# Performance work log

Measured on AMD Instinct MI355X. Metric: run time of the kernel, lower is better.

The kernel has to match this reference:

```python
import jax, jax.numpy as jnp
import numpy as np

MARGIN = 0.0
BINS = 10
ALPHA = 0.75
N = 16777216  # 2**24 pairs


def setup_inputs() -> dict:
    key = jax.random.key(0)
    k1, k2, k3 = jax.random.split(key, 3)
    output1 = jax.random.normal(k1, (N,), dtype=jnp.float32)
    output2 = jax.random.normal(k2, (N,), dtype=jnp.float32)
    target = jax.random.randint(k3, (N,), 0, 2, dtype=jnp.int64)
    return {"output1": output1, "output2": output2, "target": target}


def reference(output1, output2, target):
    dtype = output1.dtype
    t = target.astype(dtype)
    diff = output1 - output2
    # MarginRankingLoss(reduction='none'): max(0, -target*(x1-x2) + margin)
    loss = jnp.maximum(0.0, -t * diff + MARGIN)
    # gradient-norm proxy g in (0,1)
    expected_sign = 2.0 * t - 1.0
    g = jax.nn.sigmoid(-diff * expected_sign + MARGIN)
    g_norm = jnp.abs(g)
    edges = jnp.arange(BINS + 1, dtype=dtype) / BINS
    # histogram over BINS bins (fixed small loop over bins, vectorized over N)
    counts = jnp.stack([
        jnp.sum((g_norm >= edges[i]) & (g_norm < edges[i + 1]))
        for i in range(BINS)
    ]).astype(dtype)
    tot = jnp.clip(counts, 1.0)
    w = tot ** (-ALPHA)  # per-bin weight; constant wrt g in the original (.item() detaches)
    w = jax.lax.stop_gradient(w)
    bin_idx = jnp.clip(jnp.floor(g * BINS).astype(jnp.int32), 0, BINS - 1)
    sample_weights = w[bin_idx]
    return jnp.mean(loss * sample_weights)
```

## Files before the change

kernel.cpp:

```cpp
#include <hip/hip_runtime.h>

#define BINS 10
#define ALPHA 0.75f

constexpr int NB = 2048;
constexpr int NT = 256;

__global__ __launch_bounds__(NT) void ghm_pass1(
    const float* __restrict__ o1f, const float* __restrict__ o2f,
    const int* __restrict__ tgt, float* __restrict__ lsum_part,
    unsigned int* __restrict__ cnt_part, int n)
{
  const float4* o1 = reinterpret_cast<const float4*>(o1f);
  const float4* o2 = reinterpret_cast<const float4*>(o2f);
  const int4*   tg = reinterpret_cast<const int4*>(tgt);
  const int n4 = n >> 2;

  float ls[BINS];
  unsigned int c[BINS];
#pragma unroll
  for (int b = 0; b < BINS; ++b) { ls[b] = 0.0f; c[b] = 0u; }

  const int tid = blockIdx.x * NT + threadIdx.x;
  const int stride = gridDim.x * NT;

#define GHM_PROC(AX, BX, TX) do {                                   \
    float diff = (AX) - (BX);                                       \
    float tf   = (float)(TX);                                       \
    float sarg = diff * (2.0f * tf - 1.0f);                         \
    float e    = __expf(sarg);                                      \
    float g    = 1.0f / (1.0f + e);                                 \
    float loss = fmaxf(-tf * diff, 0.0f);                           \
    int bin    = (int)(g * 10.0f);                                  \
    bin = bin > (BINS - 1) ? (BINS - 1) : bin;                      \
    _Pragma("unroll")                                               \
    for (int b = 0; b < BINS; ++b) {                                \
      bool m = (bin == b);                                          \
      c[b]  += (unsigned int)m;                                     \
      ls[b] += m ? loss : 0.0f;                                     \
    }                                                               \
  } while (0)

  for (int i = tid; i < n4; i += stride) {
    float4 a  = o1[i];
    float4 bb = o2[i];
    int4   t  = tg[i];
    GHM_PROC(a.x, bb.x, t.x);
    GHM_PROC(a.y, bb.y, t.y);
    GHM_PROC(a.z, bb.z, t.z);
    GHM_PROC(a.w, bb.w, t.w);
  }
  if (tid == 0) {
    for (int i = n4 * 4; i < n; ++i) GHM_PROC(o1f[i], o2f[i], tgt[i]);
  }
#undef GHM_PROC

  const int lane = threadIdx.x & 63;
  const int wv   = threadIdx.x >> 6;
  __shared__ float        s_ls[NT / 64][BINS];
  __shared__ unsigned int s_c [NT / 64][BINS];
#pragma unroll
  for (int b = 0; b < BINS; ++b) {
    float v = ls[b];
    unsigned int cv = c[b];
#pragma unroll
    for (int off = 32; off >= 1; off >>= 1) {
      v  += __shfl_down(v, off, 64);
      cv += __shfl_down(cv, off, 64);
    }
    if (lane == 0) { s_ls[wv][b] = v; s_c[wv][b] = cv; }
  }
  __syncthreads();
  if (threadIdx.x < BINS) {
    float v = 0.0f; unsigned int cv = 0u;
#pragma unroll
    for (int w = 0; w < NT / 64; ++w) { v += s_ls[w][threadIdx.x]; cv += s_c[w][threadIdx.x]; }
    lsum_part[blockIdx.x * BINS + threadIdx.x] = v;
    cnt_part [blockIdx.x * BINS + threadIdx.x] = cv;
  }
}

__global__ __launch_bounds__(NT) void ghm_pass2(
    const float* __restrict__ lsum_part, const unsigned int* __restrict__ cnt_part,
    float* __restrict__ out, int nparts, int n)
{
  double ls[BINS];
  unsigned long long c[BINS];
#pragma unroll
  for (int b = 0; b < BINS; ++b) { ls[b] = 0.0; c[b] = 0ull; }

  for (int i = threadIdx.x; i < nparts; i += NT) {
#pragma unroll
    for (int b = 0; b < BINS; ++b) {
      ls[b] += (double)lsum_part[i * BINS + b];
      c[b]  += (unsigned long long)cnt_part[i * BINS + b];
    }
  }

  const int lane = threadIdx.x & 63;
  const int wv   = threadIdx.x >> 6;
  __shared__ double             s_ls[NT / 64][BINS];
  __shared__ unsigned long long s_c [NT / 64][BINS];
#pragma unroll
  for (int b = 0; b < BINS; ++b) {
    double v = ls[b];
    unsigned long long cv = c[b];
#pragma unroll
    for (int off = 32; off >= 1; off >>= 1) {
      v  += __shfl_down(v, off, 64);
      cv += __shfl_down(cv, off, 64);
    }
    if (lane == 0) { s_ls[wv][b] = v; s_c[wv][b] = cv; }
  }
  __syncthreads();
  if (threadIdx.x == 0) {
    double total = 0.0;
#pragma unroll
    for (int b = 0; b < BINS; ++b) {
      double lv = 0.0;
      unsigned long long cv = 0ull;
#pragma unroll
      for (int w = 0; w < NT / 64; ++w) { lv += s_ls[w][b]; cv += s_c[w][b]; }
      float cf  = (float)cv;
      float tot = fmaxf(cf, 1.0f);
      float wgt = powf(tot, -ALPHA);
      total += lv * (double)wgt;
    }
    out[0] = (float)(total / (double)n);
  }
}

extern "C" void kernel_launch(void* const* d_in, const int* in_sizes, int n_in,
                              void* d_out, int out_size, void* d_ws, size_t ws_size,
                              hipStream_t stream) {
  const float* o1  = (const float*)d_in[0];
  const float* o2  = (const float*)d_in[1];
  const int*   tgt = (const int*)d_in[2];
  float* out = (float*)d_out;
  const int n = in_sizes[0];

  int nb = NB;
  size_t need = (size_t)nb * BINS * (sizeof(float) + sizeof(unsigned int));
  while (nb > 1 && need > ws_size) { nb >>= 1; need >>= 1; }
  float* lsum_part = (float*)d_ws;
  unsigned int* cnt_part = (unsigned int*)((char*)d_ws + (size_t)nb * BINS * sizeof(float));

  ghm_pass1<<<nb, NT, 0, stream>>>(o1, o2, tgt, lsum_part, cnt_part, n);
  ghm_pass2<<<1, NT, 0, stream>>>(lsum_part, cnt_part, out, nb, n);
}
```

Before: 209.1 us.

## Replace sigmoid binning with logit-threshold cumulative counts and unrolled prefetch

```diff
diff --git a/kernel.cpp b/kernel.cpp
--- a/kernel.cpp
+++ b/kernel.cpp
@@ -3,10 +3,31 @@
 #define BINS 10
 #define ALPHA 0.75f
 
-constexpr int NB = 2048;
-constexpr int NT = 256;
+constexpr int NB    = 2048;
+constexpr int NT    = 256;
+constexpr int ITERS = 8;
+constexpr int NT2   = 1024;
 
-__global__ __launch_bounds__(NT) void ghm_pass1(
+__device__ __constant__ float LTH[9] = {
+    2.19722458f,  1.38629436f,  0.847297861f, 0.405465108f, 0.0f,
+   -0.405465108f, -0.847297861f, -1.38629436f, -2.19722458f};
+
+#define GHM_PROC(AX, BX, TX) do {                                    \
+    float diff = (AX) - (BX);                                        \
+    float nd   = -diff;                                              \
+    bool  tt   = (TX) != 0;                                          \
+    float u    = tt ? diff : nd;                                     \
+    float loss = tt ? fmaxf(nd, 0.0f) : 0.0f;                        \
+    cls[0] += loss;                                                  \
+    _Pragma("unroll")                                                \
+    for (int k = 1; k < BINS; ++k) {                                 \
+      bool p = (u <= LTH[k - 1]);                                    \
+      cls[k] += p ? loss : 0.0f;                                     \
+      cnt[k] += (unsigned int)p;                                     \
+    }                                                                \
+  } while (0)
+
+__global__ __launch_bounds__(NT, 4) void ghm_pass1(
     const float* __restrict__ o1f, const float* __restrict__ o2f,
     const int* __restrict__ tgt, float* __restrict__ lsum_part,
     unsigned int* __restrict__ cnt_part, int n)
@@ -14,46 +35,46 @@
   const float4* o1 = reinterpret_cast<const float4*>(o1f);
   const float4* o2 = reinterpret_cast<const float4*>(o2f);
   const int4*   tg = reinterpret_cast<const int4*>(tgt);
-  const int n4 = n >> 2;
 
-  float ls[BINS];
-  unsigned int c[BINS];
+  float        cls[BINS];
+  unsigned int cnt[BINS];
 #pragma unroll
-  for (int b = 0; b < BINS; ++b) { ls[b] = 0.0f; c[b] = 0u; }
+  for (int b = 0; b < BINS; ++b) { cls[b] = 0.0f; cnt[b] = 0u; }
 
-  const int tid = blockIdx.x * NT + threadIdx.x;
-  const int stride = gridDim.x * NT;
-
-#define GHM_PROC(AX, BX, TX) do {                                   \
-    float diff = (AX) - (BX);                                       \
-    float tf   = (float)(TX);                                       \
-    float sarg = diff * (2.0f * tf - 1.0f);                         \
-    float e    = __expf(sarg);                                      \
-    float g    = 1.0f / (1.0f + e);                                 \
-    float loss = fmaxf(-tf * diff, 0.0f);                           \
-    int bin    = (int)(g * 10.0f);                                  \
-    bin = bin > (BINS - 1) ? (BINS - 1) : bin;                      \
-    _Pragma("unroll")                                               \
-    for (int b = 0; b < BINS; ++b) {                                \
-      bool m = (bin == b);                                          \
-      c[b]  += (unsigned int)m;                                     \
-      ls[b] += m ? loss : 0.0f;                                     \
-    }                                                               \
-  } while (0)
-
-  for (int i = tid; i < n4; i += stride) {
-    float4 a  = o1[i];
-    float4 bb = o2[i];
-    int4   t  = tg[i];
-    GHM_PROC(a.x, bb.x, t.x);
-    GHM_PROC(a.y, bb.y, t.y);
-    GHM_PROC(a.z, bb.z, t.z);
-    GHM_PROC(a.w, bb.w, t.w);
+  if (n == NB * NT * ITERS * 4 && gridDim.x == NB) {
+    const int base = blockIdx.x * (NT * ITERS) + threadIdx.x;
+    float4 av[ITERS], bv[ITERS];
+    int4   tv[ITERS];
+#pragma unroll
+    for (int k = 0; k < ITERS; ++k) {
+      av[k] = o1[base + k * NT];
+      bv[k] = o2[base + k * NT];
+      tv[k] = tg[base + k * NT];
+    }
+#pragma unroll
+    for (int k = 0; k < ITERS; ++k) {
+      GHM_PROC(av[k].x, bv[k].x, tv[k].x);
+      GHM_PROC(av[k].y, bv[k].y, tv[k].y);
+      GHM_PROC(av[k].z, bv[k].z, tv[k].z);
+      GHM_PROC(av[k].w, bv[k].w, tv[k].w);
+    }
+  } else {
+    const int tid = blockIdx.x * NT + threadIdx.x;
+    const int stride = gridDim.x * NT;
+    const int n4 = n >> 2;
+    for (int i = tid; i < n4; i += stride) {
+      float4 a  = o1[i];
+      float4 bb = o2[i];
+      int4   t  = tg[i];
+      GHM_PROC(a.x, bb.x, t.x);
+      GHM_PROC(a.y, bb.y, t.y);
+      GHM_PROC(a.z, bb.z, t.z);
+      GHM_PROC(a.w, bb.w, t.w);
+    }
+    if (tid == 0) {
+      for (int i = n4 * 4; i < n; ++i) GHM_PROC(o1f[i], o2f[i], tgt[i]);
+    }
   }
-  if (tid == 0) {
-    for (int i = n4 * 4; i < n; ++i) GHM_PROC(o1f[i], o2f[i], tgt[i]);
-  }
-#undef GHM_PROC
 
   const int lane = threadIdx.x & 63;
   const int wv   = threadIdx.x >> 6;
@@ -61,8 +82,8 @@
   __shared__ unsigned int s_c [NT / 64][BINS];
 #pragma unroll
   for (int b = 0; b < BINS; ++b) {
-    float v = ls[b];
-    unsigned int cv = c[b];
+    float v = cls[b];
+    unsigned int cv = cnt[b];
 #pragma unroll
     for (int off = 32; off >= 1; off >>= 1) {
       v  += __shfl_down(v, off, 64);
@@ -80,31 +101,31 @@
   }
 }
 
-__global__ __launch_bounds__(NT) void ghm_pass2(
+__global__ __launch_bounds__(NT2) void ghm_pass2(
     const float* __restrict__ lsum_part, const unsigned int* __restrict__ cnt_part,
     float* __restrict__ out, int nparts, int n)
 {
-  double ls[BINS];
-  unsigned long long c[BINS];
+  double             cls[BINS];
+  unsigned long long cc [BINS];
 #pragma unroll
-  for (int b = 0; b < BINS; ++b) { ls[b] = 0.0; c[b] = 0ull; }
+  for (int b = 0; b < BINS; ++b) { cls[b] = 0.0; cc[b] = 0ull; }
 
-  for (int i = threadIdx.x; i < nparts; i += NT) {
+  for (int i = threadIdx.x; i < nparts; i += NT2) {
 #pragma unroll
     for (int b = 0; b < BINS; ++b) {
-      ls[b] += (double)lsum_part[i * BINS + b];
-      c[b]  += (unsigned long long)cnt_part[i * BINS + b];
+      cls[b] += (double)lsum_part[i * BINS + b];
+      cc[b]  += (unsigned long long)cnt_part[i * BINS + b];
     }
   }
 
   const int lane = threadIdx.x & 63;
   const int wv   = threadIdx.x >> 6;
-  __shared__ double             s_ls[NT / 64][BINS];
-  __shared__ unsigned long long s_c [NT / 64][BINS];
+  __shared__ double             s_ls[NT2 / 64][BINS];
+  __shared__ unsigned long long s_c [NT2 / 64][BINS];
 #pragma unroll
   for (int b = 0; b < BINS; ++b) {
-    double v = ls[b];
-    unsigned long long cv = c[b];
+    double v = cls[b];
+    unsigned long long cv = cc[b];
 #pragma unroll
     for (int off = 32; off >= 1; off >>= 1) {
       v  += __shfl_down(v, off, 64);
@@ -114,17 +135,27 @@
   }
   __syncthreads();
   if (threadIdx.x == 0) {
+    double             CLS[BINS + 1];
+    unsigned long long CC [BINS + 1];
+#pragma unroll
+    for (int b = 0; b < BINS; ++b) {
+      double lv = 0.0; unsigned long long cv = 0ull;
+#pragma unroll
+      for (int w = 0; w < NT2 / 64; ++w) { lv += s_ls[w][b]; cv += s_c[w][b]; }
+      CLS[b] = lv; CC[b] = cv;
+    }
+    CLS[BINS] = 0.0; CC[BINS] = 0ull;
+    CC[0] = (unsigned long long)n;
+
     double total = 0.0;
 #pragma unroll
     for (int b = 0; b < BINS; ++b) {
-      double lv = 0.0;
-      unsigned long long cv = 0ull;
-#pragma unroll
-      for (int w = 0; w < NT / 64; ++w) { lv += s_ls[w][b]; cv += s_c[w][b]; }
-      float cf  = (float)cv;
+      double lsb             = CLS[b] - CLS[b + 1];
+      unsigned long long cb  = CC[b] - CC[b + 1];
+      float cf  = (float)cb;
       float tot = fmaxf(cf, 1.0f);
       float wgt = powf(tot, -ALPHA);
-      total += lv * (double)wgt;
+      total += lsb * (double)wgt;
     }
     out[0] = (float)(total / (double)n);
   }
@@ -146,5 +177,5 @@
   unsigned int* cnt_part = (unsigned int*)((char*)d_ws + (size_t)nb * BINS * sizeof(float));
 
   ghm_pass1<<<nb, NT, 0, stream>>>(o1, o2, tgt, lsum_part, cnt_part, n);
-  ghm_pass2<<<1, NT, 0, stream>>>(lsum_part, cnt_part, out, nb, n);
+  ghm_pass2<<<1, NT2, 0, stream>>>(lsum_part, cnt_part, out, nb, n);
 }
```

Measured after the change: 215.8 us. 3.2% more time.
